# Performance work log

Hardware: AMD Instinct MI355X
Metric: run time of the kernel (lower is better)

The kernel has to match this reference:

```python
import jax, jax.numpy as jnp
import numpy as np

INPUT_DIM = 128
HIDDEN_DIM = 128
WINDOW_SIZE = 256
BLOCK_SIZE = 256
BATCH = 8
SEQ = 8192


def setup_inputs() -> dict:
    key = jax.random.key(0)
    ks = jax.random.split(key, 7)
    s = 1.0 / np.sqrt(INPUT_DIM)
    return {
        "x": jax.random.normal(ks[0], (BATCH, SEQ, INPUT_DIM), dtype=jnp.float32),
        "Wq": jax.random.normal(ks[1], (HIDDEN_DIM, INPUT_DIM), dtype=jnp.float32) * s,
        "bq": jax.random.normal(ks[2], (HIDDEN_DIM,), dtype=jnp.float32) * s,
        "Wk": jax.random.normal(ks[3], (HIDDEN_DIM, INPUT_DIM), dtype=jnp.float32) * s,
        "bk": jax.random.normal(ks[4], (HIDDEN_DIM,), dtype=jnp.float32) * s,
        "Wv": jax.random.normal(ks[5], (HIDDEN_DIM, INPUT_DIM), dtype=jnp.float32) * s,
        "bv": jax.random.normal(ks[6], (HIDDEN_DIM,), dtype=jnp.float32) * s,
    }


def reference(x, Wq, bq, Wk, bk, Wv, bv):
    B, S, D = x.shape
    bs, w = BLOCK_SIZE, WINDOW_SIZE
    nb = S // bs
    halo = w - 1
    W = bs + 2 * halo  # per-block K/V window width

    q = x @ Wq.T + bq  # [B,S,H]
    k = x @ Wk.T + bk
    v = x @ Wv.T + bv

    # Zero-pad K/V by halo on both sides. Since there is NO softmax, padded
    # zero keys give zero scores and padded zero values contribute zero —
    # this exactly reproduces the torch code's clamped window slicing.
    k_pad = jnp.pad(k, ((0, 0), (halo, halo), (0, 0)))
    v_pad = jnp.pad(v, ((0, 0), (halo, halo), (0, 0)))

    # Gather overlapping windows: [B, nb, W, H]
    starts = jnp.arange(nb) * bs  # window start in padded coords
    idx = starts[:, None] + jnp.arange(W)[None, :]  # [nb, W]
    k_win = k_pad[:, idx, :]
    v_win = v_pad[:, idx, :]

    q_blk = q.reshape(B, nb, bs, -1)  # [B, nb, bs, H]

    scale = 1.0 / jnp.sqrt(jnp.float32(D))
    attn = jnp.einsum('bnqh,bnkh->bnqk', q_blk, k_win) * scale  # no softmax
    out = jnp.einsum('bnqk,bnkh->bnqh', attn, v_win)
    return out.reshape(B, S, -1)
```

## Files before the change

### kernel.cpp

```cpp
#include <hip/hip_runtime.h>
#include <stdint.h>


#define B_ 8
#define S_ 8192

using bf16x8 = __attribute__((ext_vector_type(8))) short;
using s16x4  = __attribute__((ext_vector_type(4))) short;
using f32x16 = __attribute__((ext_vector_type(16))) float;

__device__ __forceinline__ short f2bf(float f) {
  union { float f; uint32_t u; } v; v.f = f;
  uint32_t r = v.u + 0x7fffu + ((v.u >> 16) & 1u);
  return (short)(r >> 16);
}

#define LDW 136

__global__ __launch_bounds__(256) void proj_kernel(
    const float* __restrict__ x,
    const float* __restrict__ Wq, const float* __restrict__ bq,
    const float* __restrict__ Wk, const float* __restrict__ bk,
    const float* __restrict__ Wv, const float* __restrict__ bv,
    short* __restrict__ qb, short* __restrict__ ktb, short* __restrict__ vtb)
{
  __shared__ short wl[128 * LDW];

  const int tid  = threadIdx.x;
  const int lane = tid & 63;
  const int wv   = tid >> 6;
  const int c    = lane & 31;
  const int hl   = lane >> 5;
  const int r0   = blockIdx.x * 128;
  const int b    = r0 >> 13;
  const int s0   = r0 & (S_ - 1);

  bf16x8 afrag[8];
  {
    const float* xrow = x + (size_t)(r0 + wv * 32 + c) * 128 + hl * 8;
    #pragma unroll
    for (int kst = 0; kst < 8; ++kst) {
      const float4* p = (const float4*)(xrow + kst * 16);
      float4 f0 = p[0], f1 = p[1];
      bf16x8 a;
      a[0] = f2bf(f0.x); a[1] = f2bf(f0.y); a[2] = f2bf(f0.z); a[3] = f2bf(f0.w);
      a[4] = f2bf(f1.x); a[5] = f2bf(f1.y); a[6] = f2bf(f1.z); a[7] = f2bf(f1.w);
      afrag[kst] = a;
    }
  }

  auto stageW = [&](const float* W) {
    #pragma unroll
    for (int it = 0; it < 16; ++it) {
      int l  = it * 256 + tid;
      int n  = l >> 5;
      int k4 = (l & 31) << 2;
      const float4 f = *(const float4*)(W + n * 128 + k4);
      s16x4 o;
      o[0] = f2bf(f.x); o[1] = f2bf(f.y); o[2] = f2bf(f.z); o[3] = f2bf(f.w);
      *(s16x4*)(wl + n * LDW + k4) = o;
    }
  };

  auto gemm = [&](const float* bias, f32x16* acc) {
    #pragma unroll
    for (int nt = 0; nt < 4; ++nt) {
      float bvv = bias[nt * 32 + c];
      #pragma unroll
      for (int i = 0; i < 16; ++i) acc[nt][i] = bvv;
    }
    #pragma unroll
    for (int kst = 0; kst < 8; ++kst) {
      #pragma unroll
      for (int nt = 0; nt < 4; ++nt) {
        bf16x8 bb = *(const bf16x8*)(wl + (nt * 32 + c) * LDW + kst * 16 + hl * 8);
        acc[nt] = __builtin_amdgcn_mfma_f32_32x32x16_bf16(afrag[kst], bb, acc[nt], 0, 0, 0);
      }
    }
  };

  auto writeTransposedLDS = [&](f32x16* acc) {
    #pragma unroll
    for (int nt = 0; nt < 4; ++nt) {
      int d = nt * 32 + c;
      #pragma unroll
      for (int g = 0; g < 4; ++g) {
        #pragma unroll
        for (int p = 0; p < 2; ++p) {
          int reg = g * 4 + p * 2;
          int sl  = wv * 32 + g * 8 + hl * 4 + p * 2;
          uint32_t pk = (uint32_t)(uint16_t)f2bf(acc[nt][reg]) |
                        ((uint32_t)(uint16_t)f2bf(acc[nt][reg + 1]) << 16);
          *(uint32_t*)(wl + d * LDW + sl) = pk;
        }
      }
    }
  };

  auto storeTransposed = [&](short* dst) {
    #pragma unroll
    for (int it = 0; it < 8; ++it) {
      int l  = it * 256 + tid;
      int d  = l >> 4;
      int s8 = (l & 15) << 3;
      bf16x8 vv = *(const bf16x8*)(wl + d * LDW + s8);
      *(bf16x8*)(dst + ((size_t)b * 128 + d) * S_ + s0 + s8) = vv;
    }
  };

  stageW(Wq);
  __syncthreads();
  {
    f32x16 acc[4];
    gemm(bq, acc);
    __syncthreads();
    #pragma unroll
    for (int nt = 0; nt < 4; ++nt) {
      #pragma unroll
      for (int reg = 0; reg < 16; ++reg) {
        int row = (reg & 3) + 8 * (reg >> 2) + 4 * hl;
        wl[(wv * 32 + row) * LDW + nt * 32 + c] = f2bf(acc[nt][reg]);
      }
    }
    __syncthreads();
    #pragma unroll
    for (int it = 0; it < 8; ++it) {
      int l  = it * 256 + tid;
      int s  = l >> 4;
      int d8 = (l & 15) << 3;
      bf16x8 vv = *(const bf16x8*)(wl + s * LDW + d8);
      *(bf16x8*)(qb + (size_t)(r0 + s) * 128 + d8) = vv;
    }
  }
  __syncthreads();

  stageW(Wk);
  __syncthreads();
  {
    f32x16 acc[4];
    gemm(bk, acc);
    __syncthreads();
    writeTransposedLDS(acc);
    __syncthreads();
    storeTransposed(ktb);
  }
  __syncthreads();

  stageW(Wv);
  __syncthreads();
  {
    f32x16 acc[4];
    gemm(bv, acc);
    __syncthreads();
    writeTransposedLDS(acc);
    __syncthreads();
    storeTransposed(vtb);
  }
}

#define LDC 72
#define LDM 136
#define BUFB 36864

__global__ __launch_bounds__(512) void attn_kernel(
    const short* __restrict__ qb, const short* __restrict__ ktb,
    const short* __restrict__ vtb, float* __restrict__ out)
{
  __shared__ __align__(16) char smem[2 * BUFB + BUFB];
  short* m_l  = (short*)smem;
  float* opat = (float*)(smem + 2 * BUFB);

  const int tid  = threadIdx.x;
  const int lane = tid & 63;
  const int wv   = tid >> 6;
  const int c    = lane & 31;
  const int hl   = lane >> 5;
  const int b    = blockIdx.x >> 5;
  const int n    = blockIdx.x & 31;

  const int win_lo = (n == 0) ? 0 : n * 256 - 255;
  const int win_hi = (n == 31) ? S_ : n * 256 + 511;
  const int jlo = (n == 0) ? 4 : 0;
  const int jhi = (n == 31) ? 8 : 12;
  const int cbase = n * 256 - 256;

  const short* ktb_b = ktb + (size_t)b * 128 * S_;
  const short* vtb_b = vtb + (size_t)b * 128 * S_;

  const int ht = wv >> 1;
  const int dh = wv & 1;

  const int sd  = tid >> 3;
  const int ss8 = (tid & 7) << 3;

  f32x16 macc[2];
  #pragma unroll
  for (int ntl = 0; ntl < 2; ++ntl)
    #pragma unroll
    for (int i = 0; i < 16; ++i) macc[ntl][i] = 0.f;

  auto loadChunk = [&](int c0, bf16x8* pk, bf16x8* pv) {
    #pragma unroll
    for (int it = 0; it < 2; ++it) {
      int d  = sd + it * 64;
      int sb = c0 + ss8;
      pk[it] = *(const bf16x8*)(ktb_b + (size_t)d * S_ + sb);
      pv[it] = *(const bf16x8*)(vtb_b + (size_t)d * S_ + sb);
    }
  };

  auto storeChunk = [&](int c0, short* buf, bf16x8* pk, bf16x8* pv) {
    short* ktc = buf;
    short* vtc = buf + 128 * LDC;
    int sb = c0 + ss8;
    bool edge = (sb < win_lo) || (sb + 7 >= win_hi);
    #pragma unroll
    for (int it = 0; it < 2; ++it) {
      bf16x8 kv = pk[it];
      if (edge) {
        #pragma unroll
        for (int e = 0; e < 8; ++e)
          if (sb + e < win_lo || sb + e >= win_hi) kv[e] = 0;
      }
      int d = sd + it * 64;
      *(bf16x8*)(ktc + d * LDC + ss8) = kv;
      *(bf16x8*)(vtc + d * LDC + ss8) = pv[it];
    }
  };

  auto mfmaChunk = [&](short* buf) {
    short* ktc = buf;
    short* vtc = buf + 128 * LDC;
    #pragma unroll
    for (int kst = 0; kst < 4; ++kst) {
      bf16x8 a = *(const bf16x8*)(vtc + (ht * 32 + c) * LDC + kst * 16 + hl * 8);
      #pragma unroll
      for (int ntl = 0; ntl < 2; ++ntl) {
        int nt = dh * 2 + ntl;
        bf16x8 bb = *(const bf16x8*)(ktc + (nt * 32 + c) * LDC + kst * 16 + hl * 8);
        macc[ntl] = __builtin_amdgcn_mfma_f32_32x32x16_bf16(a, bb, macc[ntl], 0, 0, 0);
      }
    }
  };

  {
    bf16x8 pk[2], pv[2];
    loadChunk(cbase + jlo * 64, pk, pv);
    storeChunk(cbase + jlo * 64, (short*)smem, pk, pv);
  }
  __syncthreads();

  for (int j = jlo; j < jhi; ++j) {
    short* cur = (short*)(smem + (size_t)(((j - jlo) & 1) ? BUFB : 0));
    short* nxt = (short*)(smem + (size_t)(((j - jlo) & 1) ? 0 : BUFB));
    bf16x8 pk[2], pv[2];
    const bool more = (j + 1 < jhi);
    if (more) loadChunk(cbase + (j + 1) * 64, pk, pv);
    mfmaChunk(cur);
    if (more) storeChunk(cbase + (j + 1) * 64, nxt, pk, pv);
    __syncthreads();
  }

  bf16x8 qf[8];
  {
    const short* q0p = qb + ((size_t)b * S_ + n * 256 + wv * 32 + c) * 128 + hl * 8;
    #pragma unroll
    for (int kst = 0; kst < 8; ++kst) qf[kst] = *(const bf16x8*)(q0p + kst * 16);
  }

  const float scale = 0.08838834764831845f;
  #pragma unroll
  for (int ntl = 0; ntl < 2; ++ntl) {
    #pragma unroll
    for (int reg = 0; reg < 16; ++reg) {
      int row = (reg & 3) + 8 * (reg >> 2) + 4 * hl;
      m_l[(ht * 32 + row) * LDM + (dh * 2 + ntl) * 32 + c] =
          f2bf(macc[ntl][reg] * scale);
    }
  }
  __syncthreads();

  f32x16 oacc[4];
  #pragma unroll
  for (int nt = 0; nt < 4; ++nt)
    #pragma unroll
    for (int i = 0; i < 16; ++i) oacc[nt][i] = 0.f;

  #pragma unroll
  for (int kst = 0; kst < 8; ++kst) {
    #pragma unroll
    for (int nt = 0; nt < 4; ++nt) {
      bf16x8 bb = *(const bf16x8*)(m_l + (nt * 32 + c) * LDM + kst * 16 + hl * 8);
      oacc[nt] = __builtin_amdgcn_mfma_f32_32x32x16_bf16(qf[kst], bb, oacc[nt], 0, 0, 0);
    }
  }

  float* patch = opat + wv * (32 * 36);
  float* outb  = out + ((size_t)b * S_ + n * 256 + wv * 32) * 128;
  #pragma unroll
  for (int nt = 0; nt < 4; ++nt) {
    #pragma unroll
    for (int reg = 0; reg < 16; ++reg) {
      int row = (reg & 3) + 8 * (reg >> 2) + 4 * hl;
      patch[row * 36 + c] = oacc[nt][reg];
    }
    #pragma unroll
    for (int p = 0; p < 4; ++p) {
      int row = p * 8 + (lane >> 3);
      float4 vv = *(const float4*)(patch + row * 36 + (lane & 7) * 4);
      *(float4*)(outb + (size_t)row * 128 + nt * 32 + (lane & 7) * 4) = vv;
    }
  }
}

extern "C" void kernel_launch(void* const* d_in, const int* in_sizes, int n_in,
                              void* d_out, int out_size, void* d_ws, size_t ws_size,
                              hipStream_t stream) {
  const float* x  = (const float*)d_in[0];
  const float* Wq = (const float*)d_in[1];
  const float* bq = (const float*)d_in[2];
  const float* Wk = (const float*)d_in[3];
  const float* bk = (const float*)d_in[4];
  const float* Wv = (const float*)d_in[5];
  const float* bv = (const float*)d_in[6];
  float* out = (float*)d_out;

  const size_t elems = (size_t)B_ * S_ * 128;
  short* qb  = (short*)d_ws;
  short* ktb = qb + elems;
  short* vtb = ktb + elems;

  proj_kernel<<<512, 256, 0, stream>>>(x, Wq, bq, Wk, bk, Wv, bv, qb, ktb, vtb);
  attn_kernel<<<256, 512, 0, stream>>>(qb, ktb, vtb, out);
}
```

Before: 124.0 us.

## Compute per-block K^T V once and sum neighbor chunks instead of recomputing windows

Because there is no softmax, each output block equals Q times a window-summed K^T V matrix. A new chunkc_kernel computes one 128x128 K^T V per 256-row chunk. attn_kernel then sums three neighbor chunks and subtracts the single out-of-window boundary rows, using edge K/V rows that proj_kernel now saves. This removes the redundant 767-wide window reduction per block, at the cost of an extra launch, an fp32 intermediate buffer in global memory, and slightly different rounding.

New measurement: 135.6 us. 9.3% more time.

```diff
diff --git a/kernel.cpp b/kernel.cpp
--- a/kernel.cpp
+++ b/kernel.cpp
@@ -13,6 +13,10 @@
   union { float f; uint32_t u; } v; v.f = f;
   uint32_t r = v.u + 0x7fffu + ((v.u >> 16) & 1u);
   return (short)(r >> 16);
+}
+__device__ __forceinline__ float bf2f(short s) {
+  union { uint32_t u; float f; } v; v.u = ((uint32_t)(uint16_t)s) << 16;
+  return v.f;
 }
 
 #define LDW 136
@@ -22,7 +26,8 @@
     const float* __restrict__ Wq, const float* __restrict__ bq,
     const float* __restrict__ Wk, const float* __restrict__ bk,
     const float* __restrict__ Wv, const float* __restrict__ bv,
-    short* __restrict__ qb, short* __restrict__ ktb, short* __restrict__ vtb)
+    short* __restrict__ qb, short* __restrict__ ktb, short* __restrict__ vtb,
+    short* __restrict__ kedge, short* __restrict__ vedge)
 {
   __shared__ short wl[128 * LDW];
 
@@ -108,6 +113,14 @@
     }
   };
 
+  auto storeEdge = [&](short* edst) {
+    if (tid < 128) {
+      size_t eo = ((size_t)b * 32 + (s0 >> 8)) * 256;
+      if ((s0 & 255) == 0) edst[eo + tid]       = wl[tid * LDW + 0];
+      else                 edst[eo + 128 + tid] = wl[tid * LDW + 127];
+    }
+  };
+
   stageW(Wq);
   __syncthreads();
   {
@@ -143,6 +156,7 @@
     writeTransposedLDS(acc);
     __syncthreads();
     storeTransposed(ktb);
+    storeEdge(kedge);
   }
   __syncthreads();
 
@@ -155,21 +169,14 @@
     writeTransposedLDS(acc);
     __syncthreads();
     storeTransposed(vtb);
-  }
-}
-
-#define LDC 72
-#define LDM 136
-#define BUFB 36864
-
-__global__ __launch_bounds__(512) void attn_kernel(
-    const short* __restrict__ qb, const short* __restrict__ ktb,
-    const short* __restrict__ vtb, float* __restrict__ out)
+    storeEdge(vedge);
+  }
+}
+
+__global__ __launch_bounds__(512) void chunkc_kernel(
+    const short* __restrict__ ktb, const short* __restrict__ vtb,
+    float* __restrict__ Cb)
 {
-  __shared__ __align__(16) char smem[2 * BUFB + BUFB];
-  short* m_l  = (short*)smem;
-  float* opat = (float*)(smem + 2 * BUFB);
-
   const int tid  = threadIdx.x;
   const int lane = tid & 63;
   const int wv   = tid >> 6;
@@ -177,106 +184,110 @@
   const int hl   = lane >> 5;
   const int b    = blockIdx.x >> 5;
   const int n    = blockIdx.x & 31;
-
-  const int win_lo = (n == 0) ? 0 : n * 256 - 255;
-  const int win_hi = (n == 31) ? S_ : n * 256 + 511;
-  const int jlo = (n == 0) ? 4 : 0;
-  const int jhi = (n == 31) ? 8 : 12;
-  const int cbase = n * 256 - 256;
-
-  const short* ktb_b = ktb + (size_t)b * 128 * S_;
-  const short* vtb_b = vtb + (size_t)b * 128 * S_;
-
-  const int ht = wv >> 1;
-  const int dh = wv & 1;
-
-  const int sd  = tid >> 3;
-  const int ss8 = (tid & 7) << 3;
-
-  f32x16 macc[2];
-  #pragma unroll
-  for (int ntl = 0; ntl < 2; ++ntl)
-    #pragma unroll
-    for (int i = 0; i < 16; ++i) macc[ntl][i] = 0.f;
-
-  auto loadChunk = [&](int c0, bf16x8* pk, bf16x8* pv) {
-    #pragma unroll
-    for (int it = 0; it < 2; ++it) {
-      int d  = sd + it * 64;
-      int sb = c0 + ss8;
-      pk[it] = *(const bf16x8*)(ktb_b + (size_t)d * S_ + sb);
-      pv[it] = *(const bf16x8*)(vtb_b + (size_t)d * S_ + sb);
-    }
-  };
-
-  auto storeChunk = [&](int c0, short* buf, bf16x8* pk, bf16x8* pv) {
-    short* ktc = buf;
-    short* vtc = buf + 128 * LDC;
-    int sb = c0 + ss8;
-    bool edge = (sb < win_lo) || (sb + 7 >= win_hi);
-    #pragma unroll
-    for (int it = 0; it < 2; ++it) {
-      bf16x8 kv = pk[it];
-      if (edge) {
-        #pragma unroll
-        for (int e = 0; e < 8; ++e)
-          if (sb + e < win_lo || sb + e >= win_hi) kv[e] = 0;
-      }
-      int d = sd + it * 64;
-      *(bf16x8*)(ktc + d * LDC + ss8) = kv;
-      *(bf16x8*)(vtc + d * LDC + ss8) = pv[it];
-    }
-  };
-
-  auto mfmaChunk = [&](short* buf) {
-    short* ktc = buf;
-    short* vtc = buf + 128 * LDC;
-    #pragma unroll
-    for (int kst = 0; kst < 4; ++kst) {
-      bf16x8 a = *(const bf16x8*)(vtc + (ht * 32 + c) * LDC + kst * 16 + hl * 8);
-      #pragma unroll
-      for (int ntl = 0; ntl < 2; ++ntl) {
-        int nt = dh * 2 + ntl;
-        bf16x8 bb = *(const bf16x8*)(ktc + (nt * 32 + c) * LDC + kst * 16 + hl * 8);
-        macc[ntl] = __builtin_amdgcn_mfma_f32_32x32x16_bf16(a, bb, macc[ntl], 0, 0, 0);
-      }
-    }
-  };
-
-  {
-    bf16x8 pk[2], pv[2];
-    loadChunk(cbase + jlo * 64, pk, pv);
-    storeChunk(cbase + jlo * 64, (short*)smem, pk, pv);
-  }
-  __syncthreads();
-
-  for (int j = jlo; j < jhi; ++j) {
-    short* cur = (short*)(smem + (size_t)(((j - jlo) & 1) ? BUFB : 0));
-    short* nxt = (short*)(smem + (size_t)(((j - jlo) & 1) ? 0 : BUFB));
-    bf16x8 pk[2], pv[2];
-    const bool more = (j + 1 < jhi);
-    if (more) loadChunk(cbase + (j + 1) * 64, pk, pv);
-    mfmaChunk(cur);
-    if (more) storeChunk(cbase + (j + 1) * 64, nxt, pk, pv);
-    __syncthreads();
-  }
-
-  bf16x8 qf[8];
-  {
-    const short* q0p = qb + ((size_t)b * S_ + n * 256 + wv * 32 + c) * 128 + hl * 8;
-    #pragma unroll
-    for (int kst = 0; kst < 8; ++kst) qf[kst] = *(const bf16x8*)(q0p + kst * 16);
-  }
-
-  const float scale = 0.08838834764831845f;
-  #pragma unroll
-  for (int ntl = 0; ntl < 2; ++ntl) {
+  const int s0   = n * 256;
+
+  const short* ap = vtb + ((size_t)b * 128 + (wv >> 1) * 32 + c) * S_ + s0 + hl * 8;
+  const short* bp = ktb + ((size_t)b * 128 + (wv & 1) * 64 + c) * S_ + s0 + hl * 8;
+
+  f32x16 acc[2];
+  #pragma unroll
+  for (int t = 0; t < 2; ++t)
+    #pragma unroll
+    for (int i = 0; i < 16; ++i) acc[t][i] = 0.f;
+
+  #pragma unroll
+  for (int kst = 0; kst < 16; ++kst) {
+    bf16x8 a  = *(const bf16x8*)(ap + kst * 16);
+    bf16x8 b0 = *(const bf16x8*)(bp + kst * 16);
+    bf16x8 b1 = *(const bf16x8*)(bp + (size_t)32 * S_ + kst * 16);
+    acc[0] = __builtin_amdgcn_mfma_f32_32x32x16_bf16(a, b0, acc[0], 0, 0, 0);
+    acc[1] = __builtin_amdgcn_mfma_f32_32x32x16_bf16(a, b1, acc[1], 0, 0, 0);
+  }
+
+  float* Cp = Cb + ((size_t)(b * 32 + n)) * 16384;
+  #pragma unroll
+  for (int t = 0; t < 2; ++t) {
     #pragma unroll
     for (int reg = 0; reg < 16; ++reg) {
       int row = (reg & 3) + 8 * (reg >> 2) + 4 * hl;
-      m_l[(ht * 32 + row) * LDM + (dh * 2 + ntl) * 32 + c] =
-          f2bf(macc[ntl][reg] * scale);
-    }
+      Cp[((wv >> 1) * 32 + row) * 128 + (wv & 1) * 64 + t * 32 + c] = acc[t][reg];
+    }
+  }
+}
+
+#define LDM 136
+
+__global__ __launch_bounds__(512) void attn_kernel(
+    const short* __restrict__ qb, const float* __restrict__ Cb,
+    const short* __restrict__ kedge, const short* __restrict__ vedge,
+    float* __restrict__ out)
+{
+  __shared__ __align__(16) short m_l[128 * LDM];
+  __shared__ __align__(16) float opat[8 * 32 * 36];
+
+  const int tid  = threadIdx.x;
+  const int lane = tid & 63;
+  const int wv   = tid >> 6;
+  const int c    = lane & 31;
+  const int hl   = lane >> 5;
+  const int b    = blockIdx.x >> 5;
+  const int n    = blockIdx.x & 31;
+
+  const int h  = tid >> 2;
+  const int dq = (tid & 3) << 5;
+
+  float m[32];
+  #pragma unroll
+  for (int i = 0; i < 32; ++i) m[i] = 0.f;
+
+  const float* Cbase = Cb + (size_t)b * 32 * 16384;
+  #pragma unroll
+  for (int dn = -1; dn <= 1; ++dn) {
+    int nn = n + dn;
+    if (nn < 0 || nn > 31) continue;
+    const float* Cp = Cbase + (size_t)nn * 16384 + h * 128 + dq;
+    #pragma unroll
+    for (int i4 = 0; i4 < 8; ++i4) {
+      float4 f = *(const float4*)(Cp + i4 * 4);
+      m[i4 * 4 + 0] += f.x; m[i4 * 4 + 1] += f.y;
+      m[i4 * 4 + 2] += f.z; m[i4 * 4 + 3] += f.w;
+    }
+  }
+  if (n > 0) {
+    const short* ke = kedge + ((size_t)(b * 32 + n - 1)) * 256;
+    const short* ve = vedge + ((size_t)(b * 32 + n - 1)) * 256;
+    float vs = bf2f(ve[h]);
+    #pragma unroll
+    for (int i8 = 0; i8 < 4; ++i8) {
+      bf16x8 kr = *(const bf16x8*)(ke + dq + i8 * 8);
+      #pragma unroll
+      for (int j = 0; j < 8; ++j) m[i8 * 8 + j] -= vs * bf2f(kr[j]);
+    }
+  }
+  if (n < 31) {
+    const short* ke = kedge + ((size_t)(b * 32 + n + 1)) * 256 + 128;
+    const short* ve = vedge + ((size_t)(b * 32 + n + 1)) * 256 + 128;
+    float vs = bf2f(ve[h]);
+    #pragma unroll
+    for (int i8 = 0; i8 < 4; ++i8) {
+      bf16x8 kr = *(const bf16x8*)(ke + dq + i8 * 8);
+      #pragma unroll
+      for (int j = 0; j < 8; ++j) m[i8 * 8 + j] -= vs * bf2f(kr[j]);
+    }
+  }
+  const float scale = 0.08838834764831845f;
+  #pragma unroll
+  for (int i = 0; i < 16; ++i) {
+    uint32_t pk = (uint32_t)(uint16_t)f2bf(m[2 * i] * scale) |
+                  ((uint32_t)(uint16_t)f2bf(m[2 * i + 1] * scale) << 16);
+    *(uint32_t*)(m_l + h * LDM + dq + 2 * i) = pk;
+  }
+
+  bf16x8 qf[8];
+  {
+    const short* q0p = qb + ((size_t)b * S_ + n * 256 + wv * 32 + c) * 128 + hl * 8;
+    #pragma unroll
+    for (int kst = 0; kst < 8; ++kst) qf[kst] = *(const bf16x8*)(q0p + kst * 16);
   }
   __syncthreads();
 
@@ -326,10 +337,15 @@
   float* out = (float*)d_out;
 
   const size_t elems = (size_t)B_ * S_ * 128;
-  short* qb  = (short*)d_ws;
-  short* ktb = qb + elems;
-  short* vtb = ktb + elems;
-
-  proj_kernel<<<512, 256, 0, stream>>>(x, Wq, bq, Wk, bk, Wv, bv, qb, ktb, vtb);
-  attn_kernel<<<256, 512, 0, stream>>>(qb, ktb, vtb, out);
-}
+  short* qb    = (short*)d_ws;
+  short* ktb   = qb + elems;
+  short* vtb   = ktb + elems;
+  float* Cb    = (float*)(vtb + elems);
+  short* kedge = (short*)(Cb + (size_t)8 * 32 * 16384);
+  short* vedge = kedge + (size_t)8 * 32 * 256;
+
+  proj_kernel<<<512, 256, 0, stream>>>(x, Wq, bq, Wk, bk, Wv, bv,
+                                       qb, ktb, vtb, kedge, vedge);
+  chunkc_kernel<<<256, 512, 0, stream>>>(ktb, vtb, Cb);
+  attn_kernel<<<256, 512, 0, stream>>>(qb, Cb, kedge, vedge, out);
+}
```
